# Kernel tuning notes

Measured on AMD Instinct MI355X. Metric: run time of the kernel, lower is better.

Reference implementation:

```python
import jax, jax.numpy as jnp
import numpy as np

N, E, IN_CH, C, H, L, NCLS = 4096, 131072, 512, 256, 4, 3, 2
DH = C // H  # MHA head dim


def _ln(x, g, b, eps=1e-5):
    mu = x.mean(-1, keepdims=True)
    var = ((x - mu) ** 2).mean(-1, keepdims=True)
    return (x - mu) * jax.lax.rsqrt(var + eps) * g + b


def _gelu(x):
    return jax.nn.gelu(x, approximate=False)  # torch nn.GELU default (erf)


def _gatv2(x, src, dst, wl, wr, att, b):
    # x: [N,C]; wl/wr: [H*C, C]; att: [H,C]; b: [C]
    xl = (x @ wl.T).reshape(N, H, C)  # source transform
    e = jax.nn.leaky_relu(xl[src] + (x @ wr.T).reshape(N, H, C)[dst], 0.2)  # [Et,H,C]
    score = jnp.einsum('ehc,hc->eh', e, att)  # [Et,H]
    m = jax.ops.segment_max(score, dst, num_segments=N)
    ex = jnp.exp(score - m[dst])
    denom = jax.ops.segment_sum(ex, dst, num_segments=N)
    alpha = ex / denom[dst]  # segment softmax over incoming edges
    out = jax.ops.segment_sum(alpha[:, :, None] * xl[src], dst, num_segments=N)
    return out.mean(axis=1) + b  # concat=False -> head mean


def _mha(x, in_w, in_b, out_w, out_b):
    qkv = x @ in_w.T + in_b  # [N,3C]
    q, k, v = [t.reshape(N, H, DH) for t in jnp.split(qkv, 3, axis=-1)]
    scores = jnp.einsum('nhd,mhd->hnm', q, k) / np.sqrt(DH)
    probs = jax.nn.softmax(scores, axis=-1)
    o = jnp.einsum('hnm,mhd->nhd', probs, v).reshape(N, C)
    return o @ out_w.T + out_b


def setup_inputs() -> dict:
    key = jax.random.key(0)
    ks = iter(jax.random.split(key, 64))
    s = lambda shape, sc=0.05: jax.random.normal(next(ks), shape, jnp.float32) * sc
    d = {
        'x': jax.random.normal(next(ks), (N, IN_CH), jnp.float32),
        'edge_index': jax.random.randint(next(ks), (2, E), 0, N, jnp.int32),
        'in_w': s((C, IN_CH)), 'in_b': jnp.zeros((C,), jnp.float32),
        'gat_wl': s((L, H * C, C)), 'gat_wr': s((L, H * C, C)),
        'gat_att': s((L, H, C)), 'gat_b': jnp.zeros((L, C), jnp.float32),
        'mha_in_w': s((L, 3 * C, C)), 'mha_in_b': jnp.zeros((L, 3 * C), jnp.float32),
        'mha_out_w': s((L, C, C)), 'mha_out_b': jnp.zeros((L, C), jnp.float32),
        'ln1_g': jnp.ones((L, C), jnp.float32), 'ln1_b': jnp.zeros((L, C), jnp.float32),
        'ln2_g': jnp.ones((L, C), jnp.float32), 'ln2_b': jnp.zeros((L, C), jnp.float32),
        'ln3_g': jnp.ones((L, C), jnp.float32), 'ln3_b': jnp.zeros((L, C), jnp.float32),
        'ffn_w1': s((L, 2 * C, C)), 'ffn_b1': jnp.zeros((L, 2 * C), jnp.float32),
        'ffn_w2': s((L, C, 2 * C)), 'ffn_b2': jnp.zeros((L, C), jnp.float32),
        'out_w1': s((C, C)), 'out_b1': jnp.zeros((C,), jnp.float32),
        'out_w2': s((NCLS, C)), 'out_b2': jnp.zeros((NCLS,), jnp.float32),
    }
    return d


def reference(x, edge_index, in_w, in_b, gat_wl, gat_wr, gat_att, gat_b,
              mha_in_w, mha_in_b, mha_out_w, mha_out_b,
              ln1_g, ln1_b, ln2_g, ln2_b, ln3_g, ln3_b,
              ffn_w1, ffn_b1, ffn_w2, ffn_b2,
              out_w1, out_b1, out_w2, out_b2):
    # add self loops (PyG GATv2Conv default)
    loop = jnp.arange(N, dtype=edge_index.dtype)
    src = jnp.concatenate([edge_index[0], loop])
    dst = jnp.concatenate([edge_index[1], loop])

    h = x @ in_w.T + in_b  # input_proj
    for l in range(L):
        local = _gatv2(h, src, dst, gat_wl[l], gat_wr[l], gat_att[l], gat_b[l])
        h = _ln(h + local, ln1_g[l], ln1_b[l])
        attn = _mha(h, mha_in_w[l], mha_in_b[l], mha_out_w[l], mha_out_b[l])
        h = _ln(h + attn, ln2_g[l], ln2_b[l])
        ffn = _gelu(h @ ffn_w1[l].T + ffn_b1[l]) @ ffn_w2[l].T + ffn_b2[l]
        h = _ln(h + ffn, ln3_g[l], ln3_b[l])
    h = _gelu(h @ out_w1.T + out_b1)
    return h @ out_w2.T + out_b2
```

## Files before the change

### kernel.cpp

```cpp
#include <hip/hip_runtime.h>
#include <cstdint>
#include <cstddef>

typedef unsigned short u16;
typedef __bf16 bf16x8 __attribute__((ext_vector_type(8)));
typedef float f32x4 __attribute__((ext_vector_type(4)));

constexpr int kN  = 4096;
constexpr int kE  = 131072;
constexpr int kET = kE + kN;
constexpr int kIn = 512;
constexpr int kC  = 256;
constexpr int kL  = 3;

constexpr int NSPLIT = 4;
constexpr int KSPAN  = kN / NSPLIT;
constexpr int NSTEP  = KSPAN / 64;

__device__ __forceinline__ u16 f2bf(float f) {
    unsigned u = __builtin_bit_cast(unsigned, f);
    u += 0x7fffu + ((u >> 16) & 1u);
    return (u16)(u >> 16);
}
__device__ __forceinline__ float bf2f(u16 s) {
    unsigned u = ((unsigned)s) << 16;
    return __builtin_bit_cast(float, u);
}
__device__ __forceinline__ float gelu_erf(float x) {
    return 0.5f * x * (1.f + erff(x * 0.70710678118654752f));
}
__device__ __forceinline__ void gload_lds16(const u16* gsrc, u16* ldst) {
    __builtin_amdgcn_global_load_lds(
        (const __attribute__((address_space(1))) unsigned int*)gsrc,
        (__attribute__((address_space(3))) unsigned int*)ldst, 16, 0, 0);
}
__device__ __forceinline__ float dpp_ror_add16(float x) {
    int t;
    t = __builtin_amdgcn_update_dpp(0, __builtin_bit_cast(int, x), 0x121, 0xf, 0xf, true);
    x += __builtin_bit_cast(float, t);
    t = __builtin_amdgcn_update_dpp(0, __builtin_bit_cast(int, x), 0x122, 0xf, 0xf, true);
    x += __builtin_bit_cast(float, t);
    t = __builtin_amdgcn_update_dpp(0, __builtin_bit_cast(int, x), 0x124, 0xf, 0xf, true);
    x += __builtin_bit_cast(float, t);
    t = __builtin_amdgcn_update_dpp(0, __builtin_bit_cast(int, x), 0x128, 0xf, 0xf, true);
    x += __builtin_bit_cast(float, t);
    return x;
}
__device__ __forceinline__ void unpack8(uint4 u, float* x) {
    x[0] = __builtin_bit_cast(float, u.x << 16);
    x[1] = __builtin_bit_cast(float, u.x & 0xffff0000u);
    x[2] = __builtin_bit_cast(float, u.y << 16);
    x[3] = __builtin_bit_cast(float, u.y & 0xffff0000u);
    x[4] = __builtin_bit_cast(float, u.z << 16);
    x[5] = __builtin_bit_cast(float, u.z & 0xffff0000u);
    x[6] = __builtin_bit_cast(float, u.w << 16);
    x[7] = __builtin_bit_cast(float, u.w & 0xffff0000u);
}

__global__ void cast_f2b(const float* __restrict__ src, u16* __restrict__ dst, int n4) {
    int i = blockIdx.x * blockDim.x + threadIdx.x;
    if (i >= n4) return;
    float4 v = ((const float4*)src)[i];
    ushort4 o;
    o.x = f2bf(v.x); o.y = f2bf(v.y); o.z = f2bf(v.z); o.w = f2bf(v.w);
    ((ushort4*)dst)[i] = o;
}

__global__ void csr_count(const int* __restrict__ ei, int* __restrict__ cnt) {
    int e = blockIdx.x * 256 + threadIdx.x;
    if (e >= kET) return;
    int d = (e < kE) ? ei[kE + e] : (e - kE);
    atomicAdd(cnt + d, 1);
}

__global__ __launch_bounds__(1024) void csr_scan(int* __restrict__ cnt_cur, int* __restrict__ off) {
    __shared__ int lds[1024];
    int t = threadIdx.x;
    int c[4], s = 0;
#pragma unroll
    for (int j = 0; j < 4; ++j) { c[j] = cnt_cur[t * 4 + j]; s += c[j]; }
    lds[t] = s;
    __syncthreads();
    for (int d = 1; d < 1024; d <<= 1) {
        int v = (t >= d) ? lds[t - d] : 0;
        __syncthreads();
        lds[t] += v;
        __syncthreads();
    }
    int excl = lds[t] - s;
#pragma unroll
    for (int j = 0; j < 4; ++j) { off[t * 4 + j] = excl; cnt_cur[t * 4 + j] = excl; excl += c[j]; }
    if (t == 1023) off[4096] = excl;
}

__global__ void csr_scatter(const int* __restrict__ ei, int* __restrict__ cur, int* __restrict__ csrc) {
    int e = blockIdx.x * 256 + threadIdx.x;
    if (e >= kET) return;
    int s, d;
    if (e < kE) { s = ei[e]; d = ei[kE + e]; } else { s = d = e - kE; }
    int pos = atomicAdd(cur + d, 1);
    csrc[pos] = s;
}

template <int BM, int K, int ACT, int WF32, int WBF16>
__global__ __launch_bounds__(256) void gemm_st(
    const u16* __restrict__ A, const u16* __restrict__ W,
    const float* __restrict__ bias, float* __restrict__ Cf,
    u16* __restrict__ Cb, int N) {
    constexpr int BK = 32;
    constexpr int NK = K / BK;
    constexpr int MF = BM / 32;
    int tid = threadIdx.x;
    int w = tid >> 6, lane = tid & 63;
    int wr = w >> 1, wc = w & 1;
    int g = lane >> 4, r = lane & 15;
    int bm = blockIdx.y * BM;
    int bn = blockIdx.x * 64;
    __shared__ __align__(16) u16 Ab[2][BM * BK];
    __shared__ __align__(16) u16 Bb[2][64 * BK];
    int srow = w * 16 + (lane >> 2);
    int scol = (lane & 3) * 8;
    auto stage = [&](int buf, int k0) {
#pragma unroll
        for (int i = 0; i < BM / 64; ++i)
            gload_lds16(A + (size_t)(bm + i * 64 + srow) * K + k0 + scol,
                        &Ab[buf][(i * 64 + w * 16) * BK]);
        gload_lds16(W + (size_t)(bn + srow) * K + k0 + scol, &Bb[buf][w * 16 * BK]);
    };
    f32x4 acc[MF][2] = {};
    stage(0, 0);
    __syncthreads();
    for (int st = 0; st < NK; ++st) {
        int cur = st & 1;
        if (st + 1 < NK) stage(cur ^ 1, (st + 1) * BK);
        const u16* Al = &Ab[cur][0];
        const u16* Bl = &Bb[cur][0];
        bf16x8 bf[2];
#pragma unroll
        for (int u = 0; u < 2; ++u)
            bf[u] = *(const bf16x8*)(Bl + (wc * 32 + u * 16 + r) * BK + g * 8);
#pragma unroll
        for (int t = 0; t < MF; ++t) {
            bf16x8 af = *(const bf16x8*)(Al + (wr * (BM / 2) + t * 16 + r) * BK + g * 8);
#pragma unroll
            for (int u = 0; u < 2; ++u)
                acc[t][u] = __builtin_amdgcn_mfma_f32_16x16x32_bf16(af, bf[u], acc[t][u], 0, 0, 0);
        }
        __syncthreads();
    }
    int r0 = bm + wr * (BM / 2) + g * 4;
    int c0 = bn + wc * 32 + r;
#pragma unroll
    for (int t = 0; t < MF; ++t)
#pragma unroll
        for (int u = 0; u < 2; ++u)
#pragma unroll
            for (int e = 0; e < 4; ++e) {
                int row = r0 + t * 16 + e, col = c0 + u * 16;
                float v = acc[t][u][e];
                if (bias) v += bias[col];
                if (ACT == 1) v = gelu_erf(v);
                if (WF32) Cf[(size_t)row * N + col] = v;
                if (WBF16) Cb[(size_t)row * N + col] = f2bf(v);
            }
}

template <int K>
__global__ __launch_bounds__(256) void gemm_128(
    const u16* __restrict__ A, const u16* __restrict__ W,
    u16* __restrict__ Cb, int N) {
    constexpr int BK = 32;
    constexpr int NK = K / BK;
    int tid = threadIdx.x;
    int w = tid >> 6, lane = tid & 63;
    int wr = w >> 1, wc = w & 1;
    int g = lane >> 4, r = lane & 15;
    int bm = blockIdx.y * 128;
    int bn = blockIdx.x * 128;
    __shared__ __align__(16) u16 Ab[2][128 * BK];
    __shared__ __align__(16) u16 Bb[2][128 * BK];
    int srd = lane >> 2;
    int schunk = ((lane & 3) ^ ((lane >> 3) & 3)) * 8;
    auto stage = [&](int buf, int k0) {
#pragma unroll
        for (int i = 0; i < 2; ++i) {
            int rowA = bm + i * 64 + w * 16 + srd;
            int rowB = bn + i * 64 + w * 16 + srd;
            gload_lds16(A + (size_t)rowA * K + k0 + schunk, &Ab[buf][(i * 64 + w * 16) * BK]);
            gload_lds16(W + (size_t)rowB * K + k0 + schunk, &Bb[buf][(i * 64 + w * 16) * BK]);
        }
    };
    f32x4 acc[4][4] = {};
    stage(0, 0);
    __syncthreads();
    int rs = (r >> 1) & 3;
    for (int st = 0; st < NK; ++st) {
        int cur = st & 1;
        if (st + 1 < NK) stage(cur ^ 1, (st + 1) * BK);
        const u16* Al = &Ab[cur][0];
        const u16* Bl = &Bb[cur][0];
        bf16x8 bf[4];
#pragma unroll
        for (int u = 0; u < 4; ++u)
            bf[u] = *(const bf16x8*)(Bl + (wc * 64 + u * 16 + r) * BK + ((g ^ rs) * 8));
#pragma unroll
        for (int t = 0; t < 4; ++t) {
            bf16x8 af = *(const bf16x8*)(Al + (wr * 64 + t * 16 + r) * BK + ((g ^ rs) * 8));
#pragma unroll
            for (int u = 0; u < 4; ++u)
                acc[t][u] = __builtin_amdgcn_mfma_f32_16x16x32_bf16(af, bf[u], acc[t][u], 0, 0, 0);
        }
        __syncthreads();
    }
#pragma unroll
    for (int t = 0; t < 4; ++t)
#pragma unroll
        for (int u = 0; u < 4; ++u)
#pragma unroll
            for (int e = 0; e < 4; ++e) {
                int row = bm + wr * 64 + t * 16 + g * 4 + e;
                int col = bn + wc * 64 + u * 16 + r;
                Cb[(size_t)row * N + col] = f2bf(acc[t][u][e]);
            }
}

template <int K>
__global__ __launch_bounds__(256) void gemm_ln(
    const u16* __restrict__ A, const u16* __restrict__ W,
    const float* __restrict__ bias,
    const float* __restrict__ lng, const float* __restrict__ lnb,
    float* __restrict__ h, u16* __restrict__ hbf) {
    constexpr int BK = 32;
    constexpr int NK = K / BK;
    int tid = threadIdx.x;
    int w = tid >> 6, lane = tid & 63;
    int g = lane >> 4, r = lane & 15;
    int bm = blockIdx.x * 32;
    __shared__ __align__(16) u16 Ab[2][32 * BK];
    __shared__ __align__(16) u16 Bb[2][256 * BK];
    __shared__ float sums[32][4][2];
    int srd = lane >> 2;
    int schunk = ((lane & 3) ^ ((lane >> 3) & 3)) * 8;
    auto stage = [&](int buf, int k0) {
        if (w < 2)
            gload_lds16(A + (size_t)(bm + w * 16 + srd) * K + k0 + schunk,
                        &Ab[buf][(w * 16) * BK]);
#pragma unroll
        for (int i = 0; i < 4; ++i)
            gload_lds16(W + (size_t)(w * 64 + i * 16 + srd) * K + k0 + schunk,
                        &Bb[buf][(w * 64 + i * 16) * BK]);
    };
    f32x4 acc[2][4] = {};
    stage(0, 0);
    __syncthreads();
    int rs = (r >> 1) & 3;
    for (int st = 0; st < NK; ++st) {
        int cur = st & 1;
        if (st + 1 < NK) stage(cur ^ 1, (st + 1) * BK);
        const u16* Al = &Ab[cur][0];
        const u16* Bl = &Bb[cur][0];
        bf16x8 bf[4];
#pragma unroll
        for (int u = 0; u < 4; ++u)
            bf[u] = *(const bf16x8*)(Bl + (w * 64 + u * 16 + r) * BK + ((g ^ rs) * 8));
#pragma unroll
        for (int t = 0; t < 2; ++t) {
            bf16x8 af = *(const bf16x8*)(Al + (t * 16 + r) * BK + ((g ^ rs) * 8));
#pragma unroll
            for (int u = 0; u < 4; ++u)
                acc[t][u] = __builtin_amdgcn_mfma_f32_16x16x32_bf16(af, bf[u], acc[t][u], 0, 0, 0);
        }
        __syncthreads();
    }
    float val[2][4][4];
#pragma unroll
    for (int t = 0; t < 2; ++t)
#pragma unroll
        for (int e = 0; e < 4; ++e) {
            int row = bm + t * 16 + g * 4 + e;
            float s1 = 0.f, s2 = 0.f;
#pragma unroll
            for (int u = 0; u < 4; ++u) {
                int col = w * 64 + u * 16 + r;
                float v = acc[t][u][e] + bias[col] + h[(size_t)row * kC + col];
                val[t][u][e] = v;
                s1 += v;
                s2 += v * v;
            }
            s1 = dpp_ror_add16(s1);
            s2 = dpp_ror_add16(s2);
            if (r == 0) {
                sums[t * 16 + g * 4 + e][w][0] = s1;
                sums[t * 16 + g * 4 + e][w][1] = s2;
            }
        }
    __syncthreads();
#pragma unroll
    for (int t = 0; t < 2; ++t)
#pragma unroll
        for (int e = 0; e < 4; ++e) {
            int lr = t * 16 + g * 4 + e;
            int row = bm + lr;
            float S1 = sums[lr][0][0] + sums[lr][1][0] + sums[lr][2][0] + sums[lr][3][0];
            float S2 = sums[lr][0][1] + sums[lr][1][1] + sums[lr][2][1] + sums[lr][3][1];
            float mu = S1 * (1.f / kC);
            float rstd = rsqrtf(S2 * (1.f / kC) - mu * mu + 1e-5f);
#pragma unroll
            for (int u = 0; u < 4; ++u) {
                int col = w * 64 + u * 16 + r;
                float y = (val[t][u][e] - mu) * rstd * lng[col] + lnb[col];
                h[(size_t)row * kC + col] = y;
                hbf[(size_t)row * kC + col] = f2bf(y);
            }
        }
}

__global__ __launch_bounds__(256) void gat_agg(
    const u16* __restrict__ xg,
    const float* __restrict__ att, const float* __restrict__ gb,
    const int* __restrict__ off, const int* __restrict__ srcs,
    const float* __restrict__ lng, const float* __restrict__ lnb,
    float* __restrict__ h, u16* __restrict__ hbf) {
    int n = blockIdx.x;
    int w = threadIdx.x >> 6, lane = threadIdx.x & 63;
    int q = lane >> 4, t = lane & 15;
    int cb = w * 256 + t * 16;

    uint4 xru0 = *(const uint4*)(xg + (size_t)n * 2048 + 1024 + cb);
    uint4 xru1 = *(const uint4*)(xg + (size_t)n * 2048 + 1024 + cb + 8);
    float xrv[16];
    unpack8(xru0, xrv); unpack8(xru1, xrv + 8);
    float att6[16], att4[16];
#pragma unroll
    for (int j = 0; j < 16; j += 4) {
        float4 a4 = *(const float4*)(att + cb + j);
        att6[j] = 0.6f * a4.x; att6[j + 1] = 0.6f * a4.y;
        att6[j + 2] = 0.6f * a4.z; att6[j + 3] = 0.6f * a4.w;
        att4[j] = (2.f / 3.f) * att6[j]; att4[j + 1] = (2.f / 3.f) * att6[j + 1];
        att4[j + 2] = (2.f / 3.f) * att6[j + 2]; att4[j + 3] = (2.f / 3.f) * att6[j + 3];
    }

    int i0 = off[n], i1 = off[n + 1];
    float m = -1e30f, ls = 0.f;
    float acc[16] = {};
    int i = i0 + q;
    uint4 p0a, p1a, p0b, p1b;
    if (i < i1) {
        int s = srcs[i];
        p0a = *(const uint4*)(xg + (size_t)s * 2048 + cb);
        p1a = *(const uint4*)(xg + (size_t)s * 2048 + cb + 8);
    }
    if (i + 4 < i1) {
        int s = srcs[i + 4];
        p0b = *(const uint4*)(xg + (size_t)s * 2048 + cb);
        p1b = *(const uint4*)(xg + (size_t)s * 2048 + cb + 8);
    }
    while (i < i1) {
        uint4 c0 = p0a, c1 = p1a;
        p0a = p0b; p1a = p1b;
        if (i + 8 < i1) {
            int s2 = srcs[i + 8];
            p0b = *(const uint4*)(xg + (size_t)s2 * 2048 + cb);
            p1b = *(const uint4*)(xg + (size_t)s2 * 2048 + cb + 8);
        }
        float x[16];
        unpack8(c0, x); unpack8(c1, x + 8);
        float p = 0.f;
#pragma unroll
        for (int j = 0; j < 16; ++j) {
            float e = x[j] + xrv[j];
            p = fmaf(att6[j], e, p);
            p = fmaf(att4[j], __builtin_fabsf(e), p);
        }
        p = dpp_ror_add16(p);
        if (p > m) {
            float c = __expf(m - p);
            ls = ls * c + 1.f;
#pragma unroll
            for (int j = 0; j < 16; ++j) acc[j] = acc[j] * c + x[j];
            m = p;
        } else {
            float pw = __expf(p - m);
            ls += pw;
#pragma unroll
            for (int j = 0; j < 16; ++j) acc[j] = fmaf(pw, x[j], acc[j]);
        }
        i += 4;
    }
    float mm = fmaxf(m, __shfl_xor(m, 16));
    mm = fmaxf(mm, __shfl_xor(mm, 32));
    float c = __expf(m - mm);
    ls *= c;
    ls += __shfl_xor(ls, 16);
    ls += __shfl_xor(ls, 32);
#pragma unroll
    for (int j = 0; j < 16; ++j) {
        float a = acc[j] * c;
        a += __shfl_xor(a, 16);
        a += __shfl_xor(a, 32);
        acc[j] = a;
    }
    float inv = 1.f / ls;
    __shared__ float red[4][256];
    __shared__ float rs[8];
    if (q == 0) {
#pragma unroll
        for (int j = 0; j < 16; ++j) red[w][t * 16 + j] = acc[j] * inv;
    }
    __syncthreads();
    int cc = threadIdx.x;
    float vsum = 0.25f * (red[0][cc] + red[1][cc] + red[2][cc] + red[3][cc]) + gb[cc];
    float v = h[(size_t)n * kC + cc] + vsum;
    float s1 = v, s2 = v * v;
    for (int d = 1; d < 64; d <<= 1) { s1 += __shfl_xor(s1, d); s2 += __shfl_xor(s2, d); }
    if (lane == 0) { rs[w] = s1; rs[4 + w] = s2; }
    __syncthreads();
    s1 = rs[0] + rs[1] + rs[2] + rs[3];
    s2 = rs[4] + rs[5] + rs[6] + rs[7];
    float mu = s1 * (1.f / kC);
    float rstd = rsqrtf(s2 * (1.f / kC) - mu * mu + 1e-5f);
    float y = (v - mu) * rstd * lng[cc] + lnb[cc];
    h[(size_t)n * kC + cc] = y;
    hbf[(size_t)n * kC + cc] = f2bf(y);
}

__global__ __launch_bounds__(256) void qkv_repack(
    const u16* __restrict__ qkvb, u16* __restrict__ Qb, u16* __restrict__ Kb,
    u16* __restrict__ VTb) {
    int h = blockIdx.y;
    int n0 = blockIdx.x * 64;
    int t = threadIdx.x;
    int nr = t >> 2, cb = (t & 3) * 16;
    const u16* src = qkvb + (size_t)(n0 + nr) * 768 + h * 64 + cb;
    u16* qd = Qb + ((size_t)h * kN + n0 + nr) * 64 + cb;
    u16* kd = Kb + ((size_t)h * kN + n0 + nr) * 64 + cb;
    __shared__ u16 lds[64][72];
    constexpr float QS = 0.125f * 1.4426950408889634f;
#pragma unroll
    for (int j = 0; j < 16; j += 4) {
        ushort4 q4 = *(const ushort4*)(src + j);
        ushort4 k4 = *(const ushort4*)(src + 256 + j);
        ushort4 v4 = *(const ushort4*)(src + 512 + j);
        ushort4 qo;
        qo.x = f2bf(bf2f(q4.x) * QS); qo.y = f2bf(bf2f(q4.y) * QS);
        qo.z = f2bf(bf2f(q4.z) * QS); qo.w = f2bf(bf2f(q4.w) * QS);
        *(ushort4*)(qd + j) = qo;
        *(ushort4*)(kd + j) = k4;
        *(ushort4*)(&lds[nr][cb + j]) = v4;
    }
    __syncthreads();
    int d = t >> 2, nb = (t & 3) * 16;
    u16* vd = VTb + ((size_t)h * 64 + d) * kN + n0 + nb;
#pragma unroll
    for (int j = 0; j < 16; j += 4) {
        ushort4 vo;
        vo.x = lds[nb + j + 0][d];
        vo.y = lds[nb + j + 1][d];
        vo.z = lds[nb + j + 2][d];
        vo.w = lds[nb + j + 3][d];
        *(ushort4*)(vd + j) = vo;
    }
}

__global__ __launch_bounds__(256, 4) void mha_mfma2(
    const u16* __restrict__ Qb, const u16* __restrict__ Kb,
    const u16* __restrict__ VTb, float* __restrict__ opart, float* __restrict__ mlpart) {
    int qt = blockIdx.x, head = blockIdx.y, sp = blockIdx.z;
    int tid = threadIdx.x;
    int w = tid >> 6, lane = tid & 63;
    int g = lane >> 4, r = lane & 15;
    int q0 = qt * 64;
    const u16* Qh = Qb + ((size_t)head * kN + q0 + w * 16) * 64;
    const u16* Kh = Kb + (size_t)head * kN * 64;
    const u16* VTh = VTb + (size_t)head * 64 * kN;
    __shared__ u16 Kt[2][64 * 64];
    __shared__ u16 Vt[2][64 * 64];
    __shared__ u16 plds[4][16 * 64];
    int srow = w * 8 + (lane >> 3);
    int schunk = ((lane & 7) ^ ((lane >> 3) & 7)) * 8;
    int kbase = sp * KSPAN;

    bf16x8 qf0 = *(const bf16x8*)(Qh + r * 64 + g * 8);
    bf16x8 qf1 = *(const bf16x8*)(Qh + r * 64 + 32 + g * 8);

    auto stage = [&](int buf, int k0) {
#pragma unroll
        for (int i = 0; i < 2; ++i) {
            int row = i * 32 + srow;
            gload_lds16(Kh + (size_t)(k0 + row) * 64 + schunk, &Kt[buf][(i * 32 + w * 8) * 64]);
            gload_lds16(VTh + (size_t)row * kN + k0 + schunk, &Vt[buf][(i * 32 + w * 8) * 64]);
        }
    };

    f32x4 o[4] = {};
    float m = -3.0e38f, l = 0.f;

    stage(0, kbase);
    __syncthreads();

    int rx = r & 7;
    for (int st = 0; st < NSTEP; ++st) {
        int cur = st & 1;
        if (st + 1 < NSTEP) stage(cur ^ 1, kbase + (st + 1) * 64);
        const u16* Kl = &Kt[cur][0];
        const u16* Vl = &Vt[cur][0];
        f32x4 stt[4] = {};
#pragma unroll
        for (int t = 0; t < 4; ++t) {
            bf16x8 kf0 = *(const bf16x8*)(Kl + (16 * t + r) * 64 + ((0 + g) ^ rx) * 8);
            bf16x8 kf1 = *(const bf16x8*)(Kl + (16 * t + r) * 64 + ((4 + g) ^ rx) * 8);
            stt[t] = __builtin_amdgcn_mfma_f32_16x16x32_bf16(kf0, qf0, stt[t], 0, 0, 0);
            stt[t] = __builtin_amdgcn_mfma_f32_16x16x32_bf16(kf1, qf1, stt[t], 0, 0, 0);
        }
        float pm = stt[0][0];
#pragma unroll
        for (int t = 0; t < 4; ++t)
#pragma unroll
            for (int e = 0; e < 4; ++e) pm = fmaxf(pm, stt[t][e]);
        pm = fmaxf(pm, __shfl_xor(pm, 16));
        pm = fmaxf(pm, __shfl_xor(pm, 32));
        if (__any(pm > m)) {
            float mn = fmaxf(m, pm);
            float corr = __builtin_amdgcn_exp2f(m - mn);
            l *= corr;
            float corrq[4];
#pragma unroll
            for (int e = 0; e < 4; ++e) corrq[e] = __shfl(corr, g * 4 + e);
#pragma unroll
            for (int dt = 0; dt < 4; ++dt)
#pragma unroll
                for (int e = 0; e < 4; ++e) o[dt][e] *= corrq[e];
            m = mn;
        }
        float ls = 0.f;
        float p[4][4];
#pragma unroll
        for (int t = 0; t < 4; ++t)
#pragma unroll
            for (int e = 0; e < 4; ++e) { p[t][e] = __builtin_amdgcn_exp2f(stt[t][e] - m); ls += p[t][e]; }
        ls += __shfl_xor(ls, 16);
        ls += __shfl_xor(ls, 32);
        l += ls;
#pragma unroll
        for (int t = 0; t < 4; ++t) {
            ushort4 pk;
            pk.x = f2bf(p[t][0]); pk.y = f2bf(p[t][1]);
            pk.z = f2bf(p[t][2]); pk.w = f2bf(p[t][3]);
            int lc = (2 * t + (g >> 1)) ^ rx;
            *(ushort4*)(&plds[w][r * 64 + lc * 8 + (g & 1) * 4]) = pk;
        }
        bf16x8 pa0 = *(const bf16x8*)(&plds[w][r * 64 + (g ^ rx) * 8]);
        bf16x8 pa1 = *(const bf16x8*)(&plds[w][r * 64 + ((4 + g) ^ rx) * 8]);
#pragma unroll
        for (int dt = 0; dt < 4; ++dt) {
            bf16x8 vf0 = *(const bf16x8*)(Vl + (dt * 16 + r) * 64 + ((0 + g) ^ rx) * 8);
            bf16x8 vf1 = *(const bf16x8*)(Vl + (dt * 16 + r) * 64 + ((4 + g) ^ rx) * 8);
            o[dt] = __builtin_amdgcn_mfma_f32_16x16x32_bf16(pa0, vf0, o[dt], 0, 0, 0);
            o[dt] = __builtin_amdgcn_mfma_f32_16x16x32_bf16(pa1, vf1, o[dt], 0, 0, 0);
        }
        __syncthreads();
    }

    size_t slot = (size_t)(head * 64 + qt) * NSPLIT + sp;
    float* ob = opart + slot * 4096;
#pragma unroll
    for (int dt = 0; dt < 4; ++dt)
#pragma unroll
        for (int e = 0; e < 4; ++e)
            ob[(w * 16 + g * 4 + e) * 64 + dt * 16 + r] = o[dt][e];
    float* mlb = mlpart + slot * 128;
    if (g == 0) { mlb[w * 16 + r] = m; mlb[64 + w * 16 + r] = l; }
}

__global__ __launch_bounds__(256) void mha_merge(
    const float* __restrict__ opart, const float* __restrict__ mlpart,
    u16* __restrict__ attnb) {
    int head = blockIdx.y;
    int q = blockIdx.x * 4 + (threadIdx.x >> 6);
    int d = threadIdx.x & 63;
    int qt = q >> 6, ql = q & 63;
    size_t sb = (size_t)(head * 64 + qt) * NSPLIT;
    float ms[NSPLIT], lsv[NSPLIT];
    float mstar = -3.0e38f;
#pragma unroll
    for (int s = 0; s < NSPLIT; ++s) {
        ms[s] = mlpart[(sb + s) * 128 + ql];
        lsv[s] = mlpart[(sb + s) * 128 + 64 + ql];
        mstar = fmaxf(mstar, ms[s]);
    }
    float acc = 0.f, lsum = 0.f;
#pragma unroll
    for (int s = 0; s < NSPLIT; ++s) {
        float wgt = __builtin_amdgcn_exp2f(ms[s] - mstar);
        lsum += lsv[s] * wgt;
        acc += opart[(sb + s) * 4096 + ql * 64 + d] * wgt;
    }
    attnb[(size_t)q * kC + head * 64 + d] = f2bf(acc / lsum);
}

__global__ __launch_bounds__(256) void final_out(
    const u16* __restrict__ tbf, const float* __restrict__ w2,
    const float* __restrict__ b2, float* __restrict__ out) {
    int row = blockIdx.x * 4 + (threadIdx.x >> 6);
    int lane = threadIdx.x & 63;
    const ushort4 tv = *(const ushort4*)(tbf + (size_t)row * 256 + lane * 4);
    float t0 = bf2f(tv.x), t1 = bf2f(tv.y), t2 = bf2f(tv.z), t3 = bf2f(tv.w);
    const float4 w0 = *(const float4*)(w2 + lane * 4);
    const float4 w1 = *(const float4*)(w2 + 256 + lane * 4);
    float d0 = t0 * w0.x + t1 * w0.y + t2 * w0.z + t3 * w0.w;
    float d1 = t0 * w1.x + t1 * w1.y + t2 * w1.z + t3 * w1.w;
    for (int d = 1; d < 64; d <<= 1) { d0 += __shfl_xor(d0, d); d1 += __shfl_xor(d1, d); }
    if (lane == 0) {
        out[(size_t)row * 2 + 0] = d0 + b2[0];
        out[(size_t)row * 2 + 1] = d1 + b2[1];
    }
}

extern "C" void kernel_launch(void* const* d_in, const int* in_sizes, int n_in,
                              void* d_out, int out_size, void* d_ws, size_t ws_size,
                              hipStream_t stream) {
    (void)in_sizes; (void)n_in; (void)out_size;
    const float* x        = (const float*)d_in[0];
    const int*   ei       = (const int*)d_in[1];
    const float* in_w     = (const float*)d_in[2];
    const float* in_b     = (const float*)d_in[3];
    const float* gat_wl   = (const float*)d_in[4];
    const float* gat_wr   = (const float*)d_in[5];
    const float* gat_att  = (const float*)d_in[6];
    const float* gat_b    = (const float*)d_in[7];
    const float* mha_in_w = (const float*)d_in[8];
    const float* mha_in_b = (const float*)d_in[9];
    const float* mha_out_w= (const float*)d_in[10];
    const float* mha_out_b= (const float*)d_in[11];
    const float* ln1_g = (const float*)d_in[12];
    const float* ln1_b = (const float*)d_in[13];
    const float* ln2_g = (const float*)d_in[14];
    const float* ln2_b = (const float*)d_in[15];
    const float* ln3_g = (const float*)d_in[16];
    const float* ln3_b = (const float*)d_in[17];
    const float* ffn_w1 = (const float*)d_in[18];
    const float* ffn_b1 = (const float*)d_in[19];
    const float* ffn_w2 = (const float*)d_in[20];
    const float* ffn_b2 = (const float*)d_in[21];
    const float* out_w1 = (const float*)d_in[22];
    const float* out_b1 = (const float*)d_in[23];
    const float* out_w2 = (const float*)d_in[24];
    const float* out_b2 = (const float*)d_in[25];
    float* out = (float*)d_out;

    char* ws = (char*)d_ws;
    size_t off = 0;
    auto alloc = [&](size_t bytes) -> void* {
        void* p = (void*)(ws + off);
        off += (bytes + 255) & ~(size_t)255;
        return p;
    };
    float* h     = (float*)alloc((size_t)kN * kC * 4);
    u16*   hbf   = (u16*)  alloc((size_t)kN * kC * 2);
    float* xlb   = (float*)alloc((size_t)kN * 1024 * 4);
    float* xrb   = (float*)alloc((size_t)kN * 1024 * 4);
    float* qkv   = (float*)alloc((size_t)kN * 768 * 4);
    float* locb  = (float*)alloc((size_t)kN * kC * 4);
    u16*   attnb = (u16*)  alloc((size_t)kN * kC * 2);
    u16*   midb  = (u16*)  alloc((size_t)kN * 512 * 2);
    u16*   tbf   = (u16*)  alloc((size_t)kN * kC * 2);
    u16*   xbf   = (u16*)  alloc((size_t)kN * kIn * 2);
    u16*   wbf   = (u16*)  alloc((size_t)3342336 * 2);
    int*   coff  = (int*)  alloc((size_t)4097 * 4);
    int*   ccur  = (int*)  alloc((size_t)4096 * 4);
    int*   csrc  = (int*)  alloc((size_t)kET * 4);
    if (ws_size < off) return;

    u16* xgbf = (u16*)xlb;
    u16* Qb  = (u16*)xlb;
    u16* Kb  = Qb + (size_t)4 * kN * 64;
    u16* VTb = Kb + (size_t)4 * kN * 64;
    u16* qkvb = (u16*)qkv;
    float* opart  = xrb;
    float* mlpart = locb;

    const size_t OFF_INW  = 0;
    const size_t OFF_GAT  = 131072;
    const size_t OFF_MIN  = 1703936;
    const size_t OFF_MOUT = 2293760;
    const size_t OFF_F1   = 2490368;
    const size_t OFF_F2   = 2883584;
    const size_t OFF_O1   = 3276800;

    auto cast = [&](const float* s, u16* d, int n) {
        int n4 = n >> 2;
        cast_f2b<<<dim3((n4 + 255) / 256), dim3(256), 0, stream>>>(s, d, n4);
    };
    cast(x, xbf, kN * kIn);
    cast(in_w, wbf + OFF_INW, kC * kIn);
    for (int l = 0; l < kL; ++l) {
        cast(gat_wl + (size_t)l * 262144, wbf + OFF_GAT + (size_t)l * 524288, 262144);
        cast(gat_wr + (size_t)l * 262144, wbf + OFF_GAT + (size_t)l * 524288 + 262144, 262144);
    }
    cast(mha_in_w, wbf + OFF_MIN, kL * 768 * kC);
    cast(mha_out_w, wbf + OFF_MOUT, kL * kC * kC);
    cast(ffn_w1, wbf + OFF_F1, kL * 512 * kC);
    cast(ffn_w2, wbf + OFF_F2, kL * kC * 512);
    cast(out_w1, wbf + OFF_O1, kC * kC);

    hipMemsetAsync(ccur, 0, 4096 * 4, stream);
    csr_count<<<dim3((kET + 255) / 256), dim3(256), 0, stream>>>(ei, ccur);
    csr_scan<<<dim3(1), dim3(1024), 0, stream>>>(ccur, coff);
    csr_scatter<<<dim3((kET + 255) / 256), dim3(256), 0, stream>>>(ei, ccur, csrc);

    gemm_st<64, 512, 0, 1, 1><<<dim3(kC / 64, kN / 64), dim3(256), 0, stream>>>(
        xbf, wbf + OFF_INW, in_b, h, hbf, kC);

    for (int l = 0; l < kL; ++l) {
        gemm_128<256><<<dim3(2048 / 128, kN / 128), dim3(256), 0, stream>>>(
            hbf, wbf + OFF_GAT + (size_t)l * 524288, xgbf, 2048);
        gat_agg<<<dim3(kN), dim3(256), 0, stream>>>(
            xgbf, gat_att + (size_t)l * 1024, gat_b + (size_t)l * kC, coff, csrc,
            ln1_g + (size_t)l * kC, ln1_b + (size_t)l * kC, h, hbf);

        gemm_st<128, 256, 0, 0, 1><<<dim3(768 / 64, kN / 128), dim3(256), 0, stream>>>(
            hbf, wbf + OFF_MIN + (size_t)l * 768 * kC, mha_in_b + (size_t)l * 768, nullptr, qkvb, 768);
        qkv_repack<<<dim3(kN / 64, 4), dim3(256), 0, stream>>>(qkvb, Qb, Kb, VTb);
        mha_mfma2<<<dim3(kN / 64, 4, NSPLIT), dim3(256), 0, stream>>>(Qb, Kb, VTb, opart, mlpart);
        mha_merge<<<dim3(kN / 4, 4), dim3(256), 0, stream>>>(opart, mlpart, attnb);
        gemm_ln<256><<<dim3(kN / 32), dim3(256), 0, stream>>>(
            attnb, wbf + OFF_MOUT + (size_t)l * kC * kC, mha_out_b + (size_t)l * kC,
            ln2_g + (size_t)l * kC, ln2_b + (size_t)l * kC, h, hbf);

        gemm_st<64, 256, 1, 0, 1><<<dim3(512 / 64, kN / 64), dim3(256), 0, stream>>>(
            hbf, wbf + OFF_F1 + (size_t)l * 512 * kC, ffn_b1 + (size_t)l * 512, nullptr, midb, 512);
        gemm_ln<512><<<dim3(kN / 32), dim3(256), 0, stream>>>(
            midb, wbf + OFF_F2 + (size_t)l * kC * 512, ffn_b2 + (size_t)l * kC,
            ln3_g + (size_t)l * kC, ln3_b + (size_t)l * kC, h, hbf);
    }

    gemm_st<64, 256, 1, 0, 1><<<dim3(kC / 64, kN / 64), dim3(256), 0, stream>>>(
        hbf, wbf + OFF_O1, out_b1, nullptr, tbf, kC);
    final_out<<<dim3(kN / 4), dim3(256), 0, stream>>>(tbf, out_w2, out_b2, out);
}
```

Measured before the change: 522.3 us.

## Fuse weight casts, fuse QKV repack into GEMM epilogue, shrink LN GEMM tiles

Replaces the many per-tensor cast launches with one cast_all kernel that routes each index to its source and destination. Adds gemm_qkv, which writes scaled Q, K and transposed V directly from the GEMM epilogue, removing the intermediate qkv buffer and the qkv_repack kernel. Templates gemm_ln on the row-tile size and launches it with 16-row tiles to get more blocks, at the cost of reloading the weight tile in each block. Splits the GAT score accumulation into four partial sums to shorten the dependency chain.

Measured after the change: 479.0 us. 8.3% less time.

```diff
diff --git a/kernel.cpp b/kernel.cpp
--- a/kernel.cpp
+++ b/kernel.cpp
@@ -57,13 +57,43 @@
     x[7] = __builtin_bit_cast(float, u.w & 0xffff0000u);
 }
 
-__global__ void cast_f2b(const float* __restrict__ src, u16* __restrict__ dst, int n4) {
-    int i = blockIdx.x * blockDim.x + threadIdx.x;
-    if (i >= n4) return;
-    float4 v = ((const float4*)src)[i];
+__global__ void cast_all(
+    const float* __restrict__ x, const float* __restrict__ in_w,
+    const float* __restrict__ gwl, const float* __restrict__ gwr,
+    const float* __restrict__ minw, const float* __restrict__ moutw,
+    const float* __restrict__ f1, const float* __restrict__ f2,
+    const float* __restrict__ o1,
+    u16* __restrict__ xbf, u16* __restrict__ wbf) {
+    int i = blockIdx.x * 256 + threadIdx.x;
+    if (i >= 1359872) return;
+    const float* s;
+    u16* dbase;
+    int sj, dj;
+    if (i < 524288) {
+        s = x; dbase = xbf; sj = i; dj = i;
+    } else if (i < 557056) {
+        s = in_w; dbase = wbf; sj = i - 524288; dj = sj;
+    } else if (i < 753664) {
+        int j = i - 557056; int l = j >> 16, wi = j & 65535;
+        s = gwl; dbase = wbf; sj = j; dj = 32768 + l * 131072 + wi;
+    } else if (i < 950272) {
+        int j = i - 753664; int l = j >> 16, wi = j & 65535;
+        s = gwr; dbase = wbf; sj = j; dj = 32768 + l * 131072 + 65536 + wi;
+    } else if (i < 1097728) {
+        s = minw; dbase = wbf; sj = i - 950272; dj = 425984 + sj;
+    } else if (i < 1146880) {
+        s = moutw; dbase = wbf; sj = i - 1097728; dj = 573440 + sj;
+    } else if (i < 1245184) {
+        s = f1; dbase = wbf; sj = i - 1146880; dj = 622592 + sj;
+    } else if (i < 1343488) {
+        s = f2; dbase = wbf; sj = i - 1245184; dj = 720896 + sj;
+    } else {
+        s = o1; dbase = wbf; sj = i - 1343488; dj = 819200 + sj;
+    }
+    float4 v = ((const float4*)s)[sj];
     ushort4 o;
     o.x = f2bf(v.x); o.y = f2bf(v.y); o.z = f2bf(v.z); o.w = f2bf(v.w);
-    ((ushort4*)dst)[i] = o;
+    ((ushort4*)dbase)[dj] = o;
 }
 
 __global__ void csr_count(const int* __restrict__ ei, int* __restrict__ cnt) {
@@ -165,6 +195,84 @@
             }
 }
 
+__global__ __launch_bounds__(256) void gemm_qkv(
+    const u16* __restrict__ A, const u16* __restrict__ W,
+    const float* __restrict__ bias,
+    u16* __restrict__ Qb, u16* __restrict__ Kb, u16* __restrict__ VTb) {
+    constexpr int BK = 32, K = 256, NK = 8, BM = 128, MF = 4;
+    int tid = threadIdx.x;
+    int w = tid >> 6, lane = tid & 63;
+    int wr = w >> 1, wc = w & 1;
+    int g = lane >> 4, r = lane & 15;
+    int bm = blockIdx.y * BM;
+    int bn = blockIdx.x * 64;
+    __shared__ __align__(16) u16 Ab[2][BM * BK];
+    __shared__ __align__(16) u16 Bb[2][64 * BK];
+    int srow = w * 16 + (lane >> 2);
+    int scol = (lane & 3) * 8;
+    auto stage = [&](int buf, int k0) {
+#pragma unroll
+        for (int i = 0; i < 2; ++i)
+            gload_lds16(A + (size_t)(bm + i * 64 + srow) * K + k0 + scol,
+                        &Ab[buf][(i * 64 + w * 16) * BK]);
+        gload_lds16(W + (size_t)(bn + srow) * K + k0 + scol, &Bb[buf][w * 16 * BK]);
+    };
+    f32x4 acc[MF][2] = {};
+    stage(0, 0);
+    __syncthreads();
+    for (int st = 0; st < NK; ++st) {
+        int cur = st & 1;
+        if (st + 1 < NK) stage(cur ^ 1, (st + 1) * BK);
+        const u16* Al = &Ab[cur][0];
+        const u16* Bl = &Bb[cur][0];
+        bf16x8 bf[2];
+#pragma unroll
+        for (int u = 0; u < 2; ++u)
+            bf[u] = *(const bf16x8*)(Bl + (wc * 32 + u * 16 + r) * BK + g * 8);
+#pragma unroll
+        for (int t = 0; t < MF; ++t) {
+            bf16x8 af = *(const bf16x8*)(Al + (wr * 64 + t * 16 + r) * BK + g * 8);
+#pragma unroll
+            for (int u = 0; u < 2; ++u)
+                acc[t][u] = __builtin_amdgcn_mfma_f32_16x16x32_bf16(af, bf[u], acc[t][u], 0, 0, 0);
+        }
+        __syncthreads();
+    }
+    constexpr float QS = 0.125f * 1.4426950408889634f;
+    int region = blockIdx.x >> 2;
+    int head = blockIdx.x & 3;
+    int r0 = bm + wr * 64 + g * 4;
+    if (region == 2) {
+#pragma unroll
+        for (int t = 0; t < MF; ++t)
+#pragma unroll
+            for (int u = 0; u < 2; ++u) {
+                int d = wc * 32 + u * 16 + r;
+                int col = bn + d;
+                ushort4 vo;
+                vo.x = f2bf(acc[t][u][0] + bias[col]);
+                vo.y = f2bf(acc[t][u][1] + bias[col]);
+                vo.z = f2bf(acc[t][u][2] + bias[col]);
+                vo.w = f2bf(acc[t][u][3] + bias[col]);
+                *(ushort4*)(VTb + ((size_t)head * 64 + d) * kN + r0 + t * 16) = vo;
+            }
+    } else {
+        u16* dst = (region == 0) ? Qb : Kb;
+        float sc = (region == 0) ? QS : 1.f;
+#pragma unroll
+        for (int t = 0; t < MF; ++t)
+#pragma unroll
+            for (int u = 0; u < 2; ++u)
+#pragma unroll
+                for (int e = 0; e < 4; ++e) {
+                    int d = wc * 32 + u * 16 + r;
+                    int row = r0 + t * 16 + e;
+                    dst[((size_t)head * kN + row) * 64 + d] =
+                        f2bf((acc[t][u][e] + bias[bn + d]) * sc);
+                }
+    }
+}
+
 template <int K>
 __global__ __launch_bounds__(256) void gemm_128(
     const u16* __restrict__ A, const u16* __restrict__ W,
@@ -224,7 +332,7 @@
             }
 }
 
-template <int K>
+template <int BM, int K>
 __global__ __launch_bounds__(256) void gemm_ln(
     const u16* __restrict__ A, const u16* __restrict__ W,
     const float* __restrict__ bias,
@@ -232,17 +340,18 @@
     float* __restrict__ h, u16* __restrict__ hbf) {
     constexpr int BK = 32;
     constexpr int NK = K / BK;
+    constexpr int MT = BM / 16;
     int tid = threadIdx.x;
     int w = tid >> 6, lane = tid & 63;
     int g = lane >> 4, r = lane & 15;
-    int bm = blockIdx.x * 32;
-    __shared__ __align__(16) u16 Ab[2][32 * BK];
+    int bm = blockIdx.x * BM;
+    __shared__ __align__(16) u16 Ab[2][BM * BK];
     __shared__ __align__(16) u16 Bb[2][256 * BK];
-    __shared__ float sums[32][4][2];
+    __shared__ float sums[BM][4][2];
     int srd = lane >> 2;
     int schunk = ((lane & 3) ^ ((lane >> 3) & 3)) * 8;
     auto stage = [&](int buf, int k0) {
-        if (w < 2)
+        if (w < MT)
             gload_lds16(A + (size_t)(bm + w * 16 + srd) * K + k0 + schunk,
                         &Ab[buf][(w * 16) * BK]);
 #pragma unroll
@@ -250,7 +359,7 @@
             gload_lds16(W + (size_t)(w * 64 + i * 16 + srd) * K + k0 + schunk,
                         &Bb[buf][(w * 64 + i * 16) * BK]);
     };
-    f32x4 acc[2][4] = {};
+    f32x4 acc[MT][4] = {};
     stage(0, 0);
     __syncthreads();
     int rs = (r >> 1) & 3;
@@ -264,7 +373,7 @@
         for (int u = 0; u < 4; ++u)
             bf[u] = *(const bf16x8*)(Bl + (w * 64 + u * 16 + r) * BK + ((g ^ rs) * 8));
 #pragma unroll
-        for (int t = 0; t < 2; ++t) {
+        for (int t = 0; t < MT; ++t) {
             bf16x8 af = *(const bf16x8*)(Al + (t * 16 + r) * BK + ((g ^ rs) * 8));
 #pragma unroll
             for (int u = 0; u < 4; ++u)
@@ -272,9 +381,9 @@
         }
         __syncthreads();
     }
-    float val[2][4][4];
-#pragma unroll
-    for (int t = 0; t < 2; ++t)
+    float val[MT][4][4];
+#pragma unroll
+    for (int t = 0; t < MT; ++t)
 #pragma unroll
         for (int e = 0; e < 4; ++e) {
             int row = bm + t * 16 + g * 4 + e;
@@ -296,7 +405,7 @@
         }
     __syncthreads();
 #pragma unroll
-    for (int t = 0; t < 2; ++t)
+    for (int t = 0; t < MT; ++t)
 #pragma unroll
         for (int e = 0; e < 4; ++e) {
             int lr = t * 16 + g * 4 + e;
@@ -365,14 +474,14 @@
         }
         float x[16];
         unpack8(c0, x); unpack8(c1, x + 8);
-        float p = 0.f;
+        float pp[4] = {0.f, 0.f, 0.f, 0.f};
 #pragma unroll
         for (int j = 0; j < 16; ++j) {
             float e = x[j] + xrv[j];
-            p = fmaf(att6[j], e, p);
-            p = fmaf(att4[j], __builtin_fabsf(e), p);
-        }
-        p = dpp_ror_add16(p);
+            pp[j & 3] = fmaf(att6[j], e, pp[j & 3]);
+            pp[j & 3] = fmaf(att4[j], __builtin_fabsf(e), pp[j & 3]);
+        }
+        float p = dpp_ror_add16((pp[0] + pp[1]) + (pp[2] + pp[3]));
         if (p > m) {
             float c = __expf(m - p);
             ls = ls * c + 1.f;
@@ -422,44 +531,6 @@
     float y = (v - mu) * rstd * lng[cc] + lnb[cc];
     h[(size_t)n * kC + cc] = y;
     hbf[(size_t)n * kC + cc] = f2bf(y);
-}
-
-__global__ __launch_bounds__(256) void qkv_repack(
-    const u16* __restrict__ qkvb, u16* __restrict__ Qb, u16* __restrict__ Kb,
-    u16* __restrict__ VTb) {
-    int h = blockIdx.y;
-    int n0 = blockIdx.x * 64;
-    int t = threadIdx.x;
-    int nr = t >> 2, cb = (t & 3) * 16;
-    const u16* src = qkvb + (size_t)(n0 + nr) * 768 + h * 64 + cb;
-    u16* qd = Qb + ((size_t)h * kN + n0 + nr) * 64 + cb;
-    u16* kd = Kb + ((size_t)h * kN + n0 + nr) * 64 + cb;
-    __shared__ u16 lds[64][72];
-    constexpr float QS = 0.125f * 1.4426950408889634f;
-#pragma unroll
-    for (int j = 0; j < 16; j += 4) {
-        ushort4 q4 = *(const ushort4*)(src + j);
-        ushort4 k4 = *(const ushort4*)(src + 256 + j);
-        ushort4 v4 = *(const ushort4*)(src + 512 + j);
-        ushort4 qo;
-        qo.x = f2bf(bf2f(q4.x) * QS); qo.y = f2bf(bf2f(q4.y) * QS);
-        qo.z = f2bf(bf2f(q4.z) * QS); qo.w = f2bf(bf2f(q4.w) * QS);
-        *(ushort4*)(qd + j) = qo;
-        *(ushort4*)(kd + j) = k4;
-        *(ushort4*)(&lds[nr][cb + j]) = v4;
-    }
-    __syncthreads();
-    int d = t >> 2, nb = (t & 3) * 16;
-    u16* vd = VTb + ((size_t)h * 64 + d) * kN + n0 + nb;
-#pragma unroll
-    for (int j = 0; j < 16; j += 4) {
-        ushort4 vo;
-        vo.x = lds[nb + j + 0][d];
-        vo.y = lds[nb + j + 1][d];
-        vo.z = lds[nb + j + 2][d];
-        vo.w = lds[nb + j + 3][d];
-        *(ushort4*)(vd + j) = vo;
-    }
 }
 
 __global__ __launch_bounds__(256, 4) void mha_mfma2(
@@ -659,7 +730,6 @@
     u16*   hbf   = (u16*)  alloc((size_t)kN * kC * 2);
     float* xlb   = (float*)alloc((size_t)kN * 1024 * 4);
     float* xrb   = (float*)alloc((size_t)kN * 1024 * 4);
-    float* qkv   = (float*)alloc((size_t)kN * 768 * 4);
     float* locb  = (float*)alloc((size_t)kN * kC * 4);
     u16*   attnb = (u16*)  alloc((size_t)kN * kC * 2);
     u16*   midb  = (u16*)  alloc((size_t)kN * 512 * 2);
@@ -675,7 +745,6 @@
     u16* Qb  = (u16*)xlb;
     u16* Kb  = Qb + (size_t)4 * kN * 64;
     u16* VTb = Kb + (size_t)4 * kN * 64;
-    u16* qkvb = (u16*)qkv;
     float* opart  = xrb;
     float* mlpart = locb;
 
@@ -687,21 +756,9 @@
     const size_t OFF_F2   = 2883584;
     const size_t OFF_O1   = 3276800;
 
-    auto cast = [&](const float* s, u16* d, int n) {
-        int n4 = n >> 2;
-        cast_f2b<<<dim3((n4 + 255) / 256), dim3(256), 0, stream>>>(s, d, n4);
-    };
-    cast(x, xbf, kN * kIn);
-    cast(in_w, wbf + OFF_INW, kC * kIn);
-    for (int l = 0; l < kL; ++l) {
-        cast(gat_wl + (size_t)l * 262144, wbf + OFF_GAT + (size_t)l * 524288, 262144);
-        cast(gat_wr + (size_t)l * 262144, wbf + OFF_GAT + (size_t)l * 524288 + 262144, 262144);
-    }
-    cast(mha_in_w, wbf + OFF_MIN, kL * 768 * kC);
-    cast(mha_out_w, wbf + OFF_MOUT, kL * kC * kC);
-    cast(ffn_w1, wbf + OFF_F1, kL * 512 * kC);
-    cast(ffn_w2, wbf + OFF_F2, kL * kC * 512);
-    cast(out_w1, wbf + OFF_O1, kC * kC);
+    cast_all<<<dim3((1359872 + 255) / 256), dim3(256), 0, stream>>>(
+        x, in_w, gat_wl, gat_wr, mha_in_w, mha_out_w, ffn_w1, ffn_w2, out_w1,
+        xbf, wbf);
 
     hipMemsetAsync(ccur, 0, 4096 * 4, stream);
     csr_count<<<dim3((kET + 255) / 256), dim3(256), 0, stream>>>(ei, ccur);
@@ -718,18 +775,18 @@
             xgbf, gat_att + (size_t)l * 1024, gat_b + (size_t)l * kC, coff, csrc,
             ln1_g + (size_t)l * kC, ln1_b + (size_t)l * kC, h, hbf);
 
-        gemm_st<128, 256, 0, 0, 1><<<dim3(768 / 64, kN / 128), dim3(256), 0, stream>>>(
-            hbf, wbf + OFF_MIN + (size_t)l * 768 * kC, mha_in_b + (size_t)l * 768, nullptr, qkvb, 768);
-        qkv_repack<<<dim3(kN / 64, 4), dim3(256), 0, stream>>>(qkvb, Qb, Kb, VTb);
+        gemm_qkv<<<dim3(768 / 64, kN / 128), dim3(256), 0, stream>>>(
+            hbf, wbf + OFF_MIN + (size_t)l * 768 * kC, mha_in_b + (size_t)l * 768,
+            Qb, Kb, VTb);
         mha_mfma2<<<dim3(kN / 64, 4, NSPLIT), dim3(256), 0, stream>>>(Qb, Kb, VTb, opart, mlpart);
         mha_merge<<<dim3(kN / 4, 4), dim3(256), 0, stream>>>(opart, mlpart, attnb);
-        gemm_ln<256><<<dim3(kN / 32), dim3(256), 0, stream>>>(
+        gemm_ln<16, 256><<<dim3(kN / 16), dim3(256), 0, stream>>>(
             attnb, wbf + OFF_MOUT + (size_t)l * kC * kC, mha_out_b + (size_t)l * kC,
             ln2_g + (size_t)l * kC, ln2_b + (size_t)l * kC, h, hbf);
 
         gemm_st<64, 256, 1, 0, 1><<<dim3(512 / 64, kN / 64), dim3(256), 0, stream>>>(
             hbf, wbf + OFF_F1 + (size_t)l * 512 * kC, ffn_b1 + (size_t)l * 512, nullptr, midb, 512);
-        gemm_ln<512><<<dim3(kN / 32), dim3(256), 0, stream>>>(
+        gemm_ln<16, 512><<<dim3(kN / 16), dim3(256), 0, stream>>>(
             midb, wbf + OFF_F2 + (size_t)l * kC * 512, ffn_b2 + (size_t)l * kC,
             ln3_g + (size_t)l * kC, ln3_b + (size_t)l * kC, h, hbf);
     }
```
